# Optimization experiments

Hardware: AMD Instinct MI355X
Metric: run time of the kernel (lower is better)

The kernel has to match this reference:

```python
import jax, jax.numpy as jnp
import numpy as np

CHANNELS = 512
KSIZE = 5


def conv1d(x, w, b, pad):
    # x: (B, Cin, T), w: (Cout, Cin, k) -> (B, Cout, T)
    y = jax.lax.conv_general_dilated(
        x, w, window_strides=(1,), padding=[(pad, pad)],
        dimension_numbers=('NCH', 'OIH', 'NCH'))
    return y + b[None, :, None]


def setup_inputs() -> dict:
    key = jax.random.key(0)
    ks = jax.random.split(key, 10)
    B, C, T, K = 16, CHANNELS, 2048, KSIZE
    s = 0.02  # conv init scale
    return {
        'x': jax.random.normal(ks[0], (B, C, T), jnp.float32),
        'offset_w': jax.random.normal(ks[1], (2 * K, C, 3), jnp.float32) * s,
        'offset_b': jnp.zeros((2 * K,), jnp.float32),
        'mod_w': jax.random.normal(ks[2], (K, C, 3), jnp.float32) * s,
        'mod_b': jnp.zeros((K,), jnp.float32),
        'weight': jax.random.normal(ks[3], (C, C, K), jnp.float32),
        'rp1_w': jax.random.normal(ks[4], (C // 2, C, 3), jnp.float32) * s,
        'rp1_b': jnp.zeros((C // 2,), jnp.float32),
        'rp2_w': jax.random.normal(ks[5], (1, C // 2, 1), jnp.float32) * s,
        'rp2_b': jnp.zeros((1,), jnp.float32),
    }


def deformable_conv1d(x, offset, modulator, weight):
    B, C, T = x.shape
    K = weight.shape[-1]
    # offset: (B, 2K, T) -> (B, T, 2, K); only component 0 is used (as in torch src)
    off = offset.reshape(B, 2, K, T).transpose(0, 3, 1, 2)[:, :, 0, :]   # (B, T, K)
    mod = modulator.reshape(B, K, T).transpose(0, 2, 1)                   # (B, T, K)
    base = jnp.arange(T, dtype=x.dtype)[None, :, None]
    kpos = (jnp.arange(K, dtype=x.dtype) - K // 2)[None, None, :]
    pos = jnp.clip(base + kpos + off, 0, T - 1)                           # (B, T, K)
    pf = jnp.clip(jnp.floor(pos).astype(jnp.int32), 0, T - 1)
    pc = jnp.clip(jnp.ceil(pos).astype(jnp.int32), 0, T - 1)
    wf = pc.astype(x.dtype) - pos    # NB: both weights are 0 at integer pos (faithful to source)
    wc = pos - pf.astype(x.dtype)
    # gather along time for all channels at once: (B, C, T, K)
    sf = jnp.take_along_axis(x, pf.reshape(B, 1, T * K), axis=2).reshape(B, C, T, K)
    sc = jnp.take_along_axis(x, pc.reshape(B, 1, T * K), axis=2).reshape(B, C, T, K)
    sampled = sf * wf[:, None] + sc * wc[:, None]
    # only diagonal weight[c, c, k] is used in the source loops
    wdiag = weight[jnp.arange(C), jnp.arange(C), :]                       # (C, K)
    return jnp.einsum('bctk,ck,btk->bct', sampled, wdiag, mod)


def reference(x, offset_w, offset_b, mod_w, mod_b, weight, rp1_w, rp1_b, rp2_w, rp2_b):
    offset = conv1d(x, offset_w, offset_b, pad=1)            # (B, 2K, T)
    modulator = jax.nn.sigmoid(conv1d(x, mod_w, mod_b, pad=1))  # (B, K, T)
    deformed = deformable_conv1d(x, offset, modulator, weight)  # (B, C, T)
    h = jax.nn.relu(conv1d(deformed, rp1_w, rp1_b, pad=1))
    strength = conv1d(h, rp2_w, rp2_b, pad=0)[:, 0, :]          # (B, T)
    return deformed, strength
```

## Files before the change

kernel.cpp:

```cpp
#include <hip/hip_runtime.h>
#include <hip/hip_bf16.h>

#define CHN 512
#define TLEN 2048
#define KSZ 5
#define BATCH 16

typedef __hip_bfloat16 bf16;
typedef short bf16x8 __attribute__((ext_vector_type(8)));
typedef float f32x4  __attribute__((ext_vector_type(4)));

#define SAMP_BYTES (BATCH*TLEN*KSZ*8)
#define W1T_ELEMS  (16*4*3*64*40)
#define W1T_BYTES  (W1T_ELEMS*2)
#define WPK_BYTES  65536
#define DT_ROWS    2050
#define DT_CHUNK   (DT_ROWS*32)
#define DT_BYTES   ((size_t)BATCH*16*DT_CHUNK*2)

__global__ __launch_bounds__(256) void kPrep(const float* __restrict__ w1,
    bf16* __restrict__ w1t, const float* __restrict__ ow,
    const float* __restrict__ mw, float* __restrict__ wpk,
    float* __restrict__ outs, const float* __restrict__ b2p,
    bf16* __restrict__ dt)
{
  int bx = blockIdx.x;
  int tidl = threadIdx.x;
  const int NP = W1T_ELEMS/256;
  if (bx < NP) {
    int idx  = bx*256 + tidl;
    int c40  = idx % 40;
    int rest = idx / 40;
    int row  = rest & 63;
    int rr   = rest >> 6;
    int r    = rr % 3;
    int cq   = rr / 3;
    int q    = cq & 3;
    int ch   = cq >> 2;
    int co   = q*64 + row;
    float v = 0.f;
    if (c40 < 32) v = w1[(size_t)co*(CHN*3) + (ch*32 + c40)*3 + r];
    w1t[idx] = __float2bfloat16(v);
  } else if (bx < NP + 64) {
    int idx = (bx - NP)*256 + tidl;
    int j = idx & 31, c = idx >> 5;
    float v = 0.f;
    if (j < 15)      { int o = j/3,  d = j - o*3;  v = ow[o*(CHN*3) + c*3 + d]; }
    else if (j < 30) { int jj = j-15; int o = jj/3, d = jj - o*3;
                       v = mw[o*(CHN*3) + c*3 + d]; }
    wpk[idx] = v;
  } else if (bx < NP + 192) {
    outs[(bx - NP - 64)*256 + tidl] = b2p[0];
  } else if (dt) {
    int z = (bx - NP - 192)*256 + tidl;
    int chunk = z >> 6;
    int row   = ((z >> 5) & 1) ? (DT_ROWS-1) : 0;
    int col   = z & 31;
    dt[(size_t)chunk*DT_CHUNK + row*32 + col] = __float2bfloat16(0.f);
  }
}

__global__ __launch_bounds__(512) void kS(const float* __restrict__ x,
    const float* __restrict__ wpk, const float* __restrict__ ob,
    const float* __restrict__ mb, float2* __restrict__ samp)
{
  int b  = blockIdx.y;
  int t0 = blockIdx.x*64;
  int tx = threadIdx.x;
  int cg = threadIdx.y;
  int t  = t0 + tx;

  __shared__ float red[8][64][10];

  float acc[10];
  #pragma unroll
  for (int i=0;i<10;++i) acc[i]=0.f;
  const float* xb = x + (size_t)b*CHN*TLEN;
  int c0 = cg*64;
  #pragma unroll 4
  for (int c=c0;c<c0+64;++c) {
    int cu = __builtin_amdgcn_readfirstlane(c);
    const float* wp = wpk + cu*32;
    const float* xr = xb + (size_t)cu*TLEN;
    float xm = (t>0)      ? xr[t-1] : 0.f;
    float xc = xr[t];
    float xp = (t<TLEN-1) ? xr[t+1] : 0.f;
    #pragma unroll
    for (int o=0;o<5;++o) {
      acc[o]   = fmaf(xm, wp[o*3+0],    acc[o]);
      acc[o]   = fmaf(xc, wp[o*3+1],    acc[o]);
      acc[o]   = fmaf(xp, wp[o*3+2],    acc[o]);
      acc[5+o] = fmaf(xm, wp[15+o*3+0], acc[5+o]);
      acc[5+o] = fmaf(xc, wp[15+o*3+1], acc[5+o]);
      acc[5+o] = fmaf(xp, wp[15+o*3+2], acc[5+o]);
    }
  }
  #pragma unroll
  for (int i=0;i<10;++i) red[cg][tx][i] = acc[i];
  __syncthreads();
  for (int s=4;s>0;s>>=1) {
    if (cg < s) {
      #pragma unroll
      for (int i=0;i<10;++i) red[cg][tx][i] += red[cg+s][tx][i];
    }
    __syncthreads();
  }
  if (cg==0) {
    #pragma unroll
    for (int k=0;k<KSZ;++k) {
      float off = red[0][tx][k]   + ob[k];
      float mv  = red[0][tx][5+k] + mb[k];
      float sig = 1.f/(1.f + expf(-mv));
      float pos = (float)(t + k - 2) + off;
      pos = fminf(fmaxf(pos, 0.f), (float)(TLEN-1));
      samp[((size_t)b*TLEN + t)*KSZ + k] = make_float2(pos, sig);
    }
  }
}

#define BT   128
#define HALO 16
#define XLEN 160

template<bool WDT>
__global__ __launch_bounds__(64) void kDf(const float* __restrict__ x,
    const float* __restrict__ wgt, const float2* __restrict__ sampg,
    float* __restrict__ out, bf16* __restrict__ dt)
{
  int b  = blockIdx.z;
  int c0 = blockIdx.y*16;
  int t0 = blockIdx.x*BT;
  int tx = threadIdx.x;

  __shared__ float xs[16*XLEN];

  int lo = min(max(t0 - HALO, 0), TLEN - XLEN);

  const float* xb = x + (size_t)b*CHN*TLEN;
  #pragma unroll
  for (int it = 0; it < 10; ++it) {
    int idx = tx + it*64;
    int c  = idx / 40;
    int c4 = idx - c*40;
    const float* src = xb + (size_t)(c0 + c)*TLEN + lo + c4*4;
    __builtin_amdgcn_global_load_lds(
        (const __attribute__((address_space(1))) unsigned int*)src,
        (__attribute__((address_space(3))) unsigned int*)&xs[idx*4],
        16, 0, 0);
  }

  int   bl[2][KSZ];
  float wf[2][KSZ], wc[2][KSZ];
  bool ok = true;
  #pragma unroll
  for (int j=0;j<2;++j)
    #pragma unroll
    for (int k=0;k<KSZ;++k) {
      float2 s = sampg[((size_t)b*TLEN + t0 + j*64 + tx)*KSZ + k];
      float pos = s.x, sig = s.y;
      float pf = floorf(pos), pc = ceilf(pos);
      int base = min((int)pf, TLEN-2);
      wf[j][k] = (pc - pos)*sig;
      wc[j][k] = (pos - pf)*sig;
      int bloc = base - lo;
      bl[j][k] = bloc;
      ok = ok && (bloc >= 0) && (bloc <= XLEN-2);
    }
  int fast = __all((int)ok);

  asm volatile("s_waitcnt vmcnt(0)" ::: "memory");
  __builtin_amdgcn_sched_barrier(0);

  unsigned pk0[8], pk1[8];
  if (fast) {
    #pragma unroll
    for (int i=0;i<16;++i) {
      int cu = __builtin_amdgcn_readfirstlane(c0 + i);
      const float* wd = wgt + (size_t)cu*(CHN*KSZ) + (size_t)cu*KSZ;
      float w0 = wd[0], w1v = wd[1], w2v = wd[2], w3 = wd[3], w4 = wd[4];
      const float* xr = xs + i*XLEN;
      float o0, o1;
      {
        float a = 0.f;
        a = fmaf(fmaf(xr[bl[0][0]+1], wc[0][0], xr[bl[0][0]]*wf[0][0]), w0,  a);
        a = fmaf(fmaf(xr[bl[0][1]+1], wc[0][1], xr[bl[0][1]]*wf[0][1]), w1v, a);
        a = fmaf(fmaf(xr[bl[0][2]+1], wc[0][2], xr[bl[0][2]]*wf[0][2]), w2v, a);
        a = fmaf(fmaf(xr[bl[0][3]+1], wc[0][3], xr[bl[0][3]]*wf[0][3]), w3,  a);
        a = fmaf(fmaf(xr[bl[0][4]+1], wc[0][4], xr[bl[0][4]]*wf[0][4]), w4,  a);
        o0 = a;
      }
      {
        float a = 0.f;
        a = fmaf(fmaf(xr[bl[1][0]+1], wc[1][0], xr[bl[1][0]]*wf[1][0]), w0,  a);
        a = fmaf(fmaf(xr[bl[1][1]+1], wc[1][1], xr[bl[1][1]]*wf[1][1]), w1v, a);
        a = fmaf(fmaf(xr[bl[1][2]+1], wc[1][2], xr[bl[1][2]]*wf[1][2]), w2v, a);
        a = fmaf(fmaf(xr[bl[1][3]+1], wc[1][3], xr[bl[1][3]]*wf[1][3]), w3,  a);
        a = fmaf(fmaf(xr[bl[1][4]+1], wc[1][4], xr[bl[1][4]]*wf[1][4]), w4,  a);
        o1 = a;
      }
      size_t op = ((size_t)b*CHN + cu)*TLEN + t0 + tx;
      out[op]      = o0;
      out[op + 64] = o1;
      if (WDT) {
        union { bf16 h; unsigned short u; } cv0, cv1;
        cv0.h = __float2bfloat16(o0);
        cv1.h = __float2bfloat16(o1);
        if (i & 1) { pk0[i>>1] |= (unsigned)cv0.u << 16;
                     pk1[i>>1] |= (unsigned)cv1.u << 16; }
        else       { pk0[i>>1]  = cv0.u;  pk1[i>>1]  = cv1.u; }
      }
    }
  } else {
    #pragma unroll
    for (int i=0;i<16;++i) {
      int cu = __builtin_amdgcn_readfirstlane(c0 + i);
      const float* wd = wgt + (size_t)cu*(CHN*KSZ) + (size_t)cu*KSZ;
      float wk0 = wd[0], wk1 = wd[1], wk2 = wd[2], wk3 = wd[3], wk4 = wd[4];
      const float* xr = xb + (size_t)cu*TLEN + lo;
      float o[2];
      #pragma unroll
      for (int j=0;j<2;++j) {
        float a = 0.f;
        a = fmaf(fmaf(xr[bl[j][0]+1], wc[j][0], xr[bl[j][0]]*wf[j][0]), wk0, a);
        a = fmaf(fmaf(xr[bl[j][1]+1], wc[j][1], xr[bl[j][1]]*wf[j][1]), wk1, a);
        a = fmaf(fmaf(xr[bl[j][2]+1], wc[j][2], xr[bl[j][2]]*wf[j][2]), wk2, a);
        a = fmaf(fmaf(xr[bl[j][3]+1], wc[j][3], xr[bl[j][3]]*wf[j][3]), wk3, a);
        a = fmaf(fmaf(xr[bl[j][4]+1], wc[j][4], xr[bl[j][4]]*wf[j][4]), wk4, a);
        o[j] = a;
      }
      size_t op = ((size_t)b*CHN + cu)*TLEN + t0 + tx;
      out[op]      = o[0];
      out[op + 64] = o[1];
      if (WDT) {
        union { bf16 h; unsigned short u; } cv0, cv1;
        cv0.h = __float2bfloat16(o[0]);
        cv1.h = __float2bfloat16(o[1]);
        if (i & 1) { pk0[i>>1] |= (unsigned)cv0.u << 16;
                     pk1[i>>1] |= (unsigned)cv1.u << 16; }
        else       { pk0[i>>1]  = cv0.u;  pk1[i>>1]  = cv1.u; }
      }
    }
  }

  if (WDT) {
    int ch   = blockIdx.y >> 1;
    int colb = (blockIdx.y & 1)*16;
    bf16* p0 = dt + (size_t)(b*16 + ch)*DT_CHUNK
                  + (size_t)(t0 + tx + 1)*32 + colb;
    *(uint4*)p0       = make_uint4(pk0[0], pk0[1], pk0[2], pk0[3]);
    *((uint4*)p0 + 1) = make_uint4(pk0[4], pk0[5], pk0[6], pk0[7]);
    bf16* p1 = p0 + 64*32;
    *(uint4*)p1       = make_uint4(pk1[0], pk1[1], pk1[2], pk1[3]);
    *((uint4*)p1 + 1) = make_uint4(pk1[4], pk1[5], pk1[6], pk1[7]);
  }
}

#define DMA_W2(dst, ch_) do {                                                  \
  const char* gs = (const char*)(w1t + (size_t)((ch_)*4 + m0)*7680);           \
  char* ld = (char*)&Ws[dst][0];                                               \
  for (int of = tid*16; of < 15360; of += 4096) {                              \
    __builtin_amdgcn_global_load_lds(                                          \
        (const __attribute__((address_space(1))) unsigned int*)(gs + of),      \
        (__attribute__((address_space(3))) unsigned int*)(ld + of), 16, 0, 0); \
  }                                                                            \
} while(0)

#define DMA_D2(dst, ch_) do {                                                  \
  const char* gs = (const char*)(dt + (size_t)(b*16 + (ch_))*DT_CHUNK          \
                                    + (size_t)t0*32);                          \
  char* ld = (char*)&Dt[dst][0];                                               \
  for (int of = tid*16; of < 16512; of += 4096) {                              \
    __builtin_amdgcn_global_load_lds(                                          \
        (const __attribute__((address_space(1))) unsigned int*)(gs + of),      \
        (__attribute__((address_space(3))) unsigned int*)(ld + of), 16, 0, 0); \
  }                                                                            \
} while(0)

#define COMPUTE2(cur) do {                                                     \
  _Pragma("unroll")                                                            \
  for (int r=0;r<3;++r) {                                                      \
    bf16x8 af[4], bfr[4];                                                      \
    _Pragma("unroll")                                                          \
    for (int mt=0;mt<4;++mt)                                                   \
      af[mt] = *(const bf16x8*)&Ws[cur][(size_t)(r*64 + mt*16 + ln15)*40 + quad*8];\
    _Pragma("unroll")                                                          \
    for (int nt=0;nt<4;++nt)                                                   \
      bfr[nt] = *(const bf16x8*)&Dt[cur][(size_t)(wN*64 + nt*16 + ln15 + r)*32 + quad*8];\
    _Pragma("unroll")                                                          \
    for (int mt=0;mt<4;++mt)                                                   \
      _Pragma("unroll")                                                        \
      for (int nt=0;nt<4;++nt)                                                 \
        acc[mt][nt] = __builtin_amdgcn_mfma_f32_16x16x32_bf16(                 \
            af[mt], bfr[nt], acc[mt][nt], 0, 0, 0);                            \
  }                                                                            \
} while(0)

__global__ __launch_bounds__(256, 2) void k2d(const bf16* __restrict__ dt,
    const bf16* __restrict__ w1t, const float* __restrict__ b1,
    const float* __restrict__ w2, float* __restrict__ outs)
{
  int n0 = blockIdx.x*256;
  int m0 = blockIdx.y;
  int b  = n0 / TLEN;
  int t0 = n0 % TLEN;
  int tid  = threadIdx.x;
  int lane = tid & 63;
  int wN   = tid >> 6;
  int ln15 = lane & 15, quad = lane >> 4;

  __shared__ bf16 Ws[2][3*64*40];
  __shared__ bf16 Dt[2][258*32];
  __shared__ float Ss[256];

  f32x4 acc[4][4];
  #pragma unroll
  for (int i=0;i<4;++i)
    #pragma unroll
    for (int j=0;j<4;++j) acc[i][j] = (f32x4){0.f,0.f,0.f,0.f};

  DMA_W2(0, 0);
  DMA_D2(0, 0);
  __syncthreads();

  for (int ch=0; ch<16; ++ch) {
    int cur = ch & 1;
    int nxt = cur ^ 1;
    if (ch < 15) {
      DMA_W2(nxt, ch+1);
      DMA_D2(nxt, ch+1);
    }
    COMPUTE2(cur);
    __syncthreads();
  }

  float part[4] = {0.f,0.f,0.f,0.f};
  #pragma unroll
  for (int mt=0;mt<4;++mt) {
    #pragma unroll
    for (int rr=0;rr<4;++rr) {
      int row = m0*64 + mt*16 + quad*4 + rr;
      float bias = b1[row];
      float wv   = w2[row];
      #pragma unroll
      for (int nt=0;nt<4;++nt) {
        float h = acc[mt][nt][rr] + bias;
        h = fmaxf(h, 0.f);
        part[nt] = fmaf(h, wv, part[nt]);
      }
    }
  }
  Ss[tid] = 0.f;
  __syncthreads();
  #pragma unroll
  for (int nt=0;nt<4;++nt)
    atomicAdd(&Ss[wN*64 + nt*16 + ln15], part[nt]);
  __syncthreads();
  atomicAdd(&outs[n0 + tid], Ss[tid]);
}

#define DMA_WSR(dst, ch_) do {                                                 \
  const char* gs = (const char*)(w1t + (size_t)((ch_)*4 + m0)*7680);           \
  char* ld = (char*)&Ws[dst][0];                                               \
  for (int of = tid*16; of < 15360; of += 4096) {                              \
    __builtin_amdgcn_global_load_lds(                                          \
        (const __attribute__((address_space(1))) unsigned int*)(gs + of),      \
        (__attribute__((address_space(3))) unsigned int*)(ld + of), 16, 0, 0); \
  }                                                                            \
} while(0)

#define LOAD_DTR(ch_) do {                                                     \
  const float* dpb = def + ((size_t)b*CHN + (ch_)*32 + g*8)*TLEN;              \
  _Pragma("unroll")                                                            \
  for (int s=0;s<4;++s) {                                                      \
    int t = t0 - 1 + tl + s*64;                                                \
    _Pragma("unroll")                                                          \
    for (int j=0;j<8;++j)                                                      \
      rg[s][j] = (t>=0 && t<TLEN) ? dpb[(size_t)j*TLEN + t] : 0.f;             \
  }                                                                            \
  if (tl < 2) {                                                                \
    int t = t0 - 1 + 256 + tl;                                                 \
    _Pragma("unroll")                                                          \
    for (int j=0;j<8;++j)                                                      \
      rt[j] = (t<TLEN) ? dpb[(size_t)j*TLEN + t] : 0.f;                        \
  }                                                                            \
} while(0)

#define WRITE_DTR(dst) do {                                                    \
  _Pragma("unroll")                                                            \
  for (int s=0;s<4;++s) {                                                      \
    bf16x8 v;                                                                  \
    _Pragma("unroll")                                                          \
    for (int j=0;j<8;++j) { union{bf16 h; short u;} cv;                        \
      cv.h = __float2bfloat16(rg[s][j]); v[j] = cv.u; }                        \
    *(bf16x8*)((char*)&Dt[dst][0] + (tl + s*64)*80 + g*16) = v;                \
  }                                                                            \
  if (tl < 2) {                                                                \
    bf16x8 v;                                                                  \
    _Pragma("unroll")                                                          \
    for (int j=0;j<8;++j) { union{bf16 h; short u;} cv;                        \
      cv.h = __float2bfloat16(rt[j]); v[j] = cv.u; }                           \
    *(bf16x8*)((char*)&Dt[dst][0] + (256 + tl)*80 + g*16) = v;                 \
  }                                                                            \
} while(0)

#define COMPUTER(cur) do {                                                     \
  _Pragma("unroll")                                                            \
  for (int r=0;r<3;++r) {                                                      \
    bf16x8 af[4], bfr[4];                                                      \
    _Pragma("unroll")                                                          \
    for (int mt=0;mt<4;++mt)                                                   \
      af[mt] = *(const bf16x8*)&Ws[cur][(size_t)(r*64 + mt*16 + ln15)*40 + quad*8];\
    _Pragma("unroll")                                                          \
    for (int nt=0;nt<4;++nt)                                                   \
      bfr[nt] = *(const bf16x8*)&Dt[cur][(size_t)(wN*64 + nt*16 + ln15 + r)*40 + quad*8];\
    _Pragma("unroll")                                                          \
    for (int mt=0;mt<4;++mt)                                                   \
      _Pragma("unroll")                                                        \
      for (int nt=0;nt<4;++nt)                                                 \
        acc[mt][nt] = __builtin_amdgcn_mfma_f32_16x16x32_bf16(                 \
            af[mt], bfr[nt], acc[mt][nt], 0, 0, 0);                            \
  }                                                                            \
} while(0)

__global__ __launch_bounds__(256, 2) void k2r(const float* __restrict__ def,
    const bf16* __restrict__ w1t, const float* __restrict__ b1,
    const float* __restrict__ w2, float* __restrict__ outs)
{
  int n0 = blockIdx.x*256;
  int m0 = blockIdx.y;
  int b  = n0 / TLEN;
  int t0 = n0 % TLEN;
  int tid  = threadIdx.x;
  int lane = tid & 63;
  int wN   = tid >> 6;
  int ln15 = lane & 15, quad = lane >> 4;

  __shared__ bf16 Ws[2][3*64*40];
  __shared__ bf16 Dt[2][258*40];
  __shared__ float Ss[256];

  int g  = tid >> 6;
  int tl = tid & 63;

  f32x4 acc[4][4];
  #pragma unroll
  for (int i=0;i<4;++i)
    #pragma unroll
    for (int j=0;j<4;++j) acc[i][j] = (f32x4){0.f,0.f,0.f,0.f};

  float rg[4][8], rt[8];
  #pragma unroll
  for (int j=0;j<8;++j) rt[j] = 0.f;

  DMA_WSR(0, 0);
  LOAD_DTR(0);
  WRITE_DTR(0);
  __syncthreads();

  for (int ch=0; ch<16; ++ch) {
    int cur = ch & 1;
    int nxt = cur ^ 1;
    if (ch < 15) {
      DMA_WSR(nxt, ch+1);
      LOAD_DTR(ch+1);
    }
    COMPUTER(cur);
    if (ch < 15)
      WRITE_DTR(nxt);
    __syncthreads();
  }

  float part[4] = {0.f,0.f,0.f,0.f};
  #pragma unroll
  for (int mt=0;mt<4;++mt) {
    #pragma unroll
    for (int rr=0;rr<4;++rr) {
      int row = m0*64 + mt*16 + quad*4 + rr;
      float bias = b1[row];
      float wv   = w2[row];
      #pragma unroll
      for (int nt=0;nt<4;++nt) {
        float h = acc[mt][nt][rr] + bias;
        h = fmaxf(h, 0.f);
        part[nt] = fmaf(h, wv, part[nt]);
      }
    }
  }
  Ss[tid] = 0.f;
  __syncthreads();
  #pragma unroll
  for (int nt=0;nt<4;++nt)
    atomicAdd(&Ss[wN*64 + nt*16 + ln15], part[nt]);
  __syncthreads();
  atomicAdd(&outs[n0 + tid], Ss[tid]);
}

extern "C" void kernel_launch(void* const* d_in, const int* in_sizes, int n_in,
                              void* d_out, int out_size, void* d_ws, size_t ws_size,
                              hipStream_t stream) {
  const float* x  = (const float*)d_in[0];
  const float* ow = (const float*)d_in[1];
  const float* ob = (const float*)d_in[2];
  const float* mw = (const float*)d_in[3];
  const float* mb = (const float*)d_in[4];
  const float* wg = (const float*)d_in[5];
  const float* w1 = (const float*)d_in[6];
  const float* b1 = (const float*)d_in[7];
  const float* w2 = (const float*)d_in[8];
  const float* b2 = (const float*)d_in[9];

  float* out_def = (float*)d_out;
  float* out_str = out_def + (size_t)BATCH*CHN*TLEN;

  float2* samp = (float2*)d_ws;
  bf16*   w1t  = (bf16*)((char*)d_ws + SAMP_BYTES);
  float*  wpk  = (float*)((char*)d_ws + SAMP_BYTES + W1T_BYTES);

  size_t need = (size_t)SAMP_BYTES + W1T_BYTES + WPK_BYTES + DT_BYTES;
  bf16* dt = (ws_size >= need)
      ? (bf16*)((char*)d_ws + SAMP_BYTES + W1T_BYTES + WPK_BYTES)
      : nullptr;

  kPrep<<<dim3(W1T_ELEMS/256 + 256), 256, 0, stream>>>(
      w1, w1t, ow, mw, wpk, out_str, b2, dt);
  kS   <<<dim3(TLEN/64, BATCH), dim3(64,8), 0, stream>>>(x, wpk, ob, mb, samp);
  if (dt) {
    kDf<true> <<<dim3(TLEN/BT, CHN/16, BATCH), 64, 0, stream>>>(
        x, wg, samp, out_def, dt);
    k2d<<<dim3(BATCH*TLEN/256, 4), 256, 0, stream>>>(dt, w1t, b1, w2, out_str);
  } else {
    kDf<false><<<dim3(TLEN/BT, CHN/16, BATCH), 64, 0, stream>>>(
        x, wg, samp, out_def, nullptr);
    k2r<<<dim3(BATCH*TLEN/256, 4), 256, 0, stream>>>(out_def, w1t, b1, w2, out_str);
  }
}
```

Measured before the change: 209.0 us.

## Process two time tiles per block with double-buffered LDS staging in kDf

Each kDf block now covers two consecutive 128-step time tiles, issuing async global-to-LDS loads for both into separate LDS buffers up front. It waits only for the first buffer (vmcnt(10)) before computing, so the second tile's load overlaps compute on the first. Sample-position loads for all four sub-rows are also hoisted ahead of the x loads. This halves the grid and doubles register use and LDS per block, which may reduce occupancy and latency hiding across blocks.

Result: slower. 227.4 us (+8.8%).

```diff
diff --git a/kernel.cpp b/kernel.cpp
--- a/kernel.cpp
+++ b/kernel.cpp
@@ -129,35 +129,54 @@
 {
   int b  = blockIdx.z;
   int c0 = blockIdx.y*16;
-  int t0 = blockIdx.x*BT;
+  int tA = blockIdx.x*(2*BT);
+  int tB = tA + BT;
   int tx = threadIdx.x;
 
-  __shared__ float xs[16*XLEN];
-
-  int lo = min(max(t0 - HALO, 0), TLEN - XLEN);
+  __shared__ float xs[2][16*XLEN];
+
+  int loA = min(max(tA - HALO, 0), TLEN - XLEN);
+  int loB = min(max(tB - HALO, 0), TLEN - XLEN);
+
+  float2 sv[4][KSZ];
+  #pragma unroll
+  for (int j=0;j<4;++j)
+    #pragma unroll
+    for (int k=0;k<KSZ;++k)
+      sv[j][k] = sampg[((size_t)b*TLEN + tA + j*64 + tx)*KSZ + k];
+  __builtin_amdgcn_sched_barrier(0);
 
   const float* xb = x + (size_t)b*CHN*TLEN;
   #pragma unroll
   for (int it = 0; it < 10; ++it) {
     int idx = tx + it*64;
-    int c  = idx / 40;
-    int c4 = idx - c*40;
-    const float* src = xb + (size_t)(c0 + c)*TLEN + lo + c4*4;
+    int c  = idx / 40, c4 = idx - c*40;
     __builtin_amdgcn_global_load_lds(
-        (const __attribute__((address_space(1))) unsigned int*)src,
-        (__attribute__((address_space(3))) unsigned int*)&xs[idx*4],
+        (const __attribute__((address_space(1))) unsigned int*)
+          (xb + (size_t)(c0 + c)*TLEN + loA + c4*4),
+        (__attribute__((address_space(3))) unsigned int*)&xs[0][idx*4],
         16, 0, 0);
   }
-
-  int   bl[2][KSZ];
-  float wf[2][KSZ], wc[2][KSZ];
+  #pragma unroll
+  for (int it = 0; it < 10; ++it) {
+    int idx = tx + it*64;
+    int c  = idx / 40, c4 = idx - c*40;
+    __builtin_amdgcn_global_load_lds(
+        (const __attribute__((address_space(1))) unsigned int*)
+          (xb + (size_t)(c0 + c)*TLEN + loB + c4*4),
+        (__attribute__((address_space(3))) unsigned int*)&xs[1][idx*4],
+        16, 0, 0);
+  }
+
+  int   bl[4][KSZ];
+  float wf[4][KSZ], wc[4][KSZ];
   bool ok = true;
   #pragma unroll
-  for (int j=0;j<2;++j)
+  for (int j=0;j<4;++j) {
+    int lo = (j<2) ? loA : loB;
     #pragma unroll
     for (int k=0;k<KSZ;++k) {
-      float2 s = sampg[((size_t)b*TLEN + t0 + j*64 + tx)*KSZ + k];
-      float pos = s.x, sig = s.y;
+      float pos = sv[j][k].x, sig = sv[j][k].y;
       float pf = floorf(pos), pc = ceilf(pos);
       int base = min((int)pf, TLEN-2);
       wf[j][k] = (pc - pos)*sig;
@@ -166,19 +185,20 @@
       bl[j][k] = bloc;
       ok = ok && (bloc >= 0) && (bloc <= XLEN-2);
     }
+  }
   int fast = __all((int)ok);
 
-  asm volatile("s_waitcnt vmcnt(0)" ::: "memory");
-  __builtin_amdgcn_sched_barrier(0);
-
-  unsigned pk0[8], pk1[8];
   if (fast) {
+    asm volatile("s_waitcnt vmcnt(10)" ::: "memory");
+    __builtin_amdgcn_sched_barrier(0);
+
+    unsigned pk0[8], pk1[8];
     #pragma unroll
     for (int i=0;i<16;++i) {
       int cu = __builtin_amdgcn_readfirstlane(c0 + i);
       const float* wd = wgt + (size_t)cu*(CHN*KSZ) + (size_t)cu*KSZ;
       float w0 = wd[0], w1v = wd[1], w2v = wd[2], w3 = wd[3], w4 = wd[4];
-      const float* xr = xs + i*XLEN;
+      const float* xr = &xs[0][i*XLEN];
       float o0, o1;
       {
         float a = 0.f;
@@ -198,7 +218,7 @@
         a = fmaf(fmaf(xr[bl[1][4]+1], wc[1][4], xr[bl[1][4]]*wf[1][4]), w4,  a);
         o1 = a;
       }
-      size_t op = ((size_t)b*CHN + cu)*TLEN + t0 + tx;
+      size_t op = ((size_t)b*CHN + cu)*TLEN + tA + tx;
       out[op]      = o0;
       out[op + 64] = o1;
       if (WDT) {
@@ -210,48 +230,118 @@
         else       { pk0[i>>1]  = cv0.u;  pk1[i>>1]  = cv1.u; }
       }
     }
-  } else {
+    int ch, colb;
+    if (WDT) {
+      ch   = blockIdx.y >> 1;
+      colb = (blockIdx.y & 1)*16;
+      bf16* p0 = dt + (size_t)(b*16 + ch)*DT_CHUNK
+                    + (size_t)(tA + tx + 1)*32 + colb;
+      *(uint4*)p0       = make_uint4(pk0[0], pk0[1], pk0[2], pk0[3]);
+      *((uint4*)p0 + 1) = make_uint4(pk0[4], pk0[5], pk0[6], pk0[7]);
+      bf16* p1 = p0 + 64*32;
+      *(uint4*)p1       = make_uint4(pk1[0], pk1[1], pk1[2], pk1[3]);
+      *((uint4*)p1 + 1) = make_uint4(pk1[4], pk1[5], pk1[6], pk1[7]);
+    }
+
+    asm volatile("s_waitcnt vmcnt(0)" ::: "memory");
+    __builtin_amdgcn_sched_barrier(0);
+
     #pragma unroll
     for (int i=0;i<16;++i) {
       int cu = __builtin_amdgcn_readfirstlane(c0 + i);
       const float* wd = wgt + (size_t)cu*(CHN*KSZ) + (size_t)cu*KSZ;
-      float wk0 = wd[0], wk1 = wd[1], wk2 = wd[2], wk3 = wd[3], wk4 = wd[4];
-      const float* xr = xb + (size_t)cu*TLEN + lo;
-      float o[2];
-      #pragma unroll
-      for (int j=0;j<2;++j) {
+      float w0 = wd[0], w1v = wd[1], w2v = wd[2], w3 = wd[3], w4 = wd[4];
+      const float* xr = &xs[1][i*XLEN];
+      float o0, o1;
+      {
         float a = 0.f;
-        a = fmaf(fmaf(xr[bl[j][0]+1], wc[j][0], xr[bl[j][0]]*wf[j][0]), wk0, a);
-        a = fmaf(fmaf(xr[bl[j][1]+1], wc[j][1], xr[bl[j][1]]*wf[j][1]), wk1, a);
-        a = fmaf(fmaf(xr[bl[j][2]+1], wc[j][2], xr[bl[j][2]]*wf[j][2]), wk2, a);
-        a = fmaf(fmaf(xr[bl[j][3]+1], wc[j][3], xr[bl[j][3]]*wf[j][3]), wk3, a);
-        a = fmaf(fmaf(xr[bl[j][4]+1], wc[j][4], xr[bl[j][4]]*wf[j][4]), wk4, a);
-        o[j] = a;
-      }
-      size_t op = ((size_t)b*CHN + cu)*TLEN + t0 + tx;
-      out[op]      = o[0];
-      out[op + 64] = o[1];
+        a = fmaf(fmaf(xr[bl[2][0]+1], wc[2][0], xr[bl[2][0]]*wf[2][0]), w0,  a);
+        a = fmaf(fmaf(xr[bl[2][1]+1], wc[2][1], xr[bl[2][1]]*wf[2][1]), w1v, a);
+        a = fmaf(fmaf(xr[bl[2][2]+1], wc[2][2], xr[bl[2][2]]*wf[2][2]), w2v, a);
+        a = fmaf(fmaf(xr[bl[2][3]+1], wc[2][3], xr[bl[2][3]]*wf[2][3]), w3,  a);
+        a = fmaf(fmaf(xr[bl[2][4]+1], wc[2][4], xr[bl[2][4]]*wf[2][4]), w4,  a);
+        o0 = a;
+      }
+      {
+        float a = 0.f;
+        a = fmaf(fmaf(xr[bl[3][0]+1], wc[3][0], xr[bl[3][0]]*wf[3][0]), w0,  a);
+        a = fmaf(fmaf(xr[bl[3][1]+1], wc[3][1], xr[bl[3][1]]*wf[3][1]), w1v, a);
+        a = fmaf(fmaf(xr[bl[3][2]+1], wc[3][2], xr[bl[3][2]]*wf[3][2]), w2v, a);
+        a = fmaf(fmaf(xr[bl[3][3]+1], wc[3][3], xr[bl[3][3]]*wf[3][3]), w3,  a);
+        a = fmaf(fmaf(xr[bl[3][4]+1], wc[3][4], xr[bl[3][4]]*wf[3][4]), w4,  a);
+        o1 = a;
+      }
+      size_t op = ((size_t)b*CHN + cu)*TLEN + tB + tx;
+      out[op]      = o0;
+      out[op + 64] = o1;
       if (WDT) {
         union { bf16 h; unsigned short u; } cv0, cv1;
-        cv0.h = __float2bfloat16(o[0]);
-        cv1.h = __float2bfloat16(o[1]);
+        cv0.h = __float2bfloat16(o0);
+        cv1.h = __float2bfloat16(o1);
         if (i & 1) { pk0[i>>1] |= (unsigned)cv0.u << 16;
                      pk1[i>>1] |= (unsigned)cv1.u << 16; }
         else       { pk0[i>>1]  = cv0.u;  pk1[i>>1]  = cv1.u; }
       }
     }
-  }
-
-  if (WDT) {
-    int ch   = blockIdx.y >> 1;
-    int colb = (blockIdx.y & 1)*16;
-    bf16* p0 = dt + (size_t)(b*16 + ch)*DT_CHUNK
-                  + (size_t)(t0 + tx + 1)*32 + colb;
-    *(uint4*)p0       = make_uint4(pk0[0], pk0[1], pk0[2], pk0[3]);
-    *((uint4*)p0 + 1) = make_uint4(pk0[4], pk0[5], pk0[6], pk0[7]);
-    bf16* p1 = p0 + 64*32;
-    *(uint4*)p1       = make_uint4(pk1[0], pk1[1], pk1[2], pk1[3]);
-    *((uint4*)p1 + 1) = make_uint4(pk1[4], pk1[5], pk1[6], pk1[7]);
+    if (WDT) {
+      bf16* p0 = dt + (size_t)(b*16 + ch)*DT_CHUNK
+                    + (size_t)(tB + tx + 1)*32 + colb;
+      *(uint4*)p0       = make_uint4(pk0[0], pk0[1], pk0[2], pk0[3]);
+      *((uint4*)p0 + 1) = make_uint4(pk0[4], pk0[5], pk0[6], pk0[7]);
+      bf16* p1 = p0 + 64*32;
+      *(uint4*)p1       = make_uint4(pk1[0], pk1[1], pk1[2], pk1[3]);
+      *((uint4*)p1 + 1) = make_uint4(pk1[4], pk1[5], pk1[6], pk1[7]);
+    }
+  } else {
+    asm volatile("s_waitcnt vmcnt(0)" ::: "memory");
+    __builtin_amdgcn_sched_barrier(0);
+    unsigned pk0[8], pk1[8];
+    #pragma unroll
+    for (int jj=0;jj<2;++jj) {
+      int tb = (jj==0) ? tA : tB;
+      int lo = (jj==0) ? loA : loB;
+      #pragma unroll
+      for (int i=0;i<16;++i) {
+        int cu = __builtin_amdgcn_readfirstlane(c0 + i);
+        const float* wd = wgt + (size_t)cu*(CHN*KSZ) + (size_t)cu*KSZ;
+        float wk0 = wd[0], wk1 = wd[1], wk2 = wd[2], wk3 = wd[3], wk4 = wd[4];
+        const float* xr = xb + (size_t)cu*TLEN + lo;
+        float o[2];
+        #pragma unroll
+        for (int j2=0;j2<2;++j2) {
+          int j = jj*2 + j2;
+          float a = 0.f;
+          a = fmaf(fmaf(xr[bl[j][0]+1], wc[j][0], xr[bl[j][0]]*wf[j][0]), wk0, a);
+          a = fmaf(fmaf(xr[bl[j][1]+1], wc[j][1], xr[bl[j][1]]*wf[j][1]), wk1, a);
+          a = fmaf(fmaf(xr[bl[j][2]+1], wc[j][2], xr[bl[j][2]]*wf[j][2]), wk2, a);
+          a = fmaf(fmaf(xr[bl[j][3]+1], wc[j][3], xr[bl[j][3]]*wf[j][3]), wk3, a);
+          a = fmaf(fmaf(xr[bl[j][4]+1], wc[j][4], xr[bl[j][4]]*wf[j][4]), wk4, a);
+          o[j2] = a;
+        }
+        size_t op = ((size_t)b*CHN + cu)*TLEN + tb + tx;
+        out[op]      = o[0];
+        out[op + 64] = o[1];
+        if (WDT) {
+          union { bf16 h; unsigned short u; } cv0, cv1;
+          cv0.h = __float2bfloat16(o[0]);
+          cv1.h = __float2bfloat16(o[1]);
+          if (i & 1) { pk0[i>>1] |= (unsigned)cv0.u << 16;
+                       pk1[i>>1] |= (unsigned)cv1.u << 16; }
+          else       { pk0[i>>1]  = cv0.u;  pk1[i>>1]  = cv1.u; }
+        }
+      }
+      if (WDT) {
+        int ch   = blockIdx.y >> 1;
+        int colb = (blockIdx.y & 1)*16;
+        bf16* p0 = dt + (size_t)(b*16 + ch)*DT_CHUNK
+                      + (size_t)(tb + tx + 1)*32 + colb;
+        *(uint4*)p0       = make_uint4(pk0[0], pk0[1], pk0[2], pk0[3]);
+        *((uint4*)p0 + 1) = make_uint4(pk0[4], pk0[5], pk0[6], pk0[7]);
+        bf16* p1 = p0 + 64*32;
+        *(uint4*)p1       = make_uint4(pk1[0], pk1[1], pk1[2], pk1[3]);
+        *((uint4*)p1 + 1) = make_uint4(pk1[4], pk1[5], pk1[6], pk1[7]);
+      }
+    }
   }
 }
 
@@ -525,11 +615,11 @@
       w1, w1t, ow, mw, wpk, out_str, b2, dt);
   kS   <<<dim3(TLEN/64, BATCH), dim3(64,8), 0, stream>>>(x, wpk, ob, mb, samp);
   if (dt) {
-    kDf<true> <<<dim3(TLEN/BT, CHN/16, BATCH), 64, 0, stream>>>(
+    kDf<true> <<<dim3(TLEN/(2*BT), CHN/16, BATCH), 64, 0, stream>>>(
         x, wg, samp, out_def, dt);
     k2d<<<dim3(BATCH*TLEN/256, 4), 256, 0, stream>>>(dt, w1t, b1, w2, out_str);
   } else {
-    kDf<false><<<dim3(TLEN/BT, CHN/16, BATCH), 64, 0, stream>>>(
+    kDf<false><<<dim3(TLEN/(2*BT), CHN/16, BATCH), 64, 0, stream>>>(
         x, wg, samp, out_def, nullptr);
     k2r<<<dim3(BATCH*TLEN/256, 4), 256, 0, stream>>>(out_def, w1t, b1, w2, out_str);
   }
```
